# Kernel tuning notes

Measured on AMD Instinct MI355X. Metric: run time of the kernel, lower is better.

The kernel has to match this reference:

```python
import jax, jax.numpy as jnp
import numpy as np

N_NODES = 50000
N_EDGES = 600000
IN_DIM = 128
LATENT = 128
OUT_DIM = 40
NUM_LAYERS = 2


def setup_inputs() -> dict:
    key = jax.random.key(0)
    ks = jax.random.split(key, 8)
    nodes_feats = jax.random.normal(ks[0], (N_NODES, IN_DIM), dtype=jnp.float32)
    adj_list = jax.random.randint(ks[1], (N_EDGES, 2), 0, N_NODES, dtype=jnp.int64)
    s_in = 1.0 / np.sqrt(IN_DIM)
    s_cb = 1.0 / np.sqrt(2 * LATENT)
    s_out = 1.0 / np.sqrt(LATENT)
    W_in = jax.random.uniform(ks[2], (IN_DIM, LATENT), jnp.float32, -s_in, s_in)
    b_in = jnp.zeros((LATENT,), jnp.float32)
    W_comb = jax.random.uniform(ks[3], (NUM_LAYERS, 2 * LATENT, LATENT), jnp.float32, -s_cb, s_cb)
    b_comb = jnp.zeros((NUM_LAYERS, LATENT), jnp.float32)
    W_out = jax.random.uniform(ks[4], (LATENT, OUT_DIM), jnp.float32, -s_out, s_out)
    b_out = jnp.zeros((OUT_DIM,), jnp.float32)
    return {"nodes_feats": nodes_feats, "adj_list": adj_list, "W_in": W_in, "b_in": b_in,
            "W_comb": W_comb, "b_comb": b_comb, "W_out": W_out, "b_out": b_out}


def reference(nodes_feats, adj_list, W_in, b_in, W_comb, b_comb, W_out, b_out):
    n = nodes_feats.shape[0]
    fro = adj_list[:, 0]
    to = adj_list[:, 1]
    # initialize: project input features to latent space
    h = jax.nn.relu(nodes_feats @ W_in + b_in)  # [N, LATENT]
    # in-degree for mean aggregation (replaces per-node Python stack+mean)
    deg = jax.ops.segment_sum(jnp.ones(fro.shape[0], h.dtype), to, num_segments=n)
    inv_deg = 1.0 / jnp.maximum(deg, 1.0)  # guard isolated nodes
    for l in range(W_comb.shape[0]):
        # gather neighbor feats along edges, scatter-add to destinations, mean
        msg = jax.ops.segment_sum(h[fro], to, num_segments=n) * inv_deg[:, None]
        # combine: ReLU(Linear([node || message]))
        h = jax.nn.relu(jnp.concatenate([h, msg], axis=-1) @ W_comb[l] + b_comb[l])
    # output head (logits for CrossEntropyLoss)
    return h @ W_out + b_out
```

## Files before the change

### kernel.cpp

```cpp
#include <hip/hip_runtime.h>
#include <hip/hip_fp16.h>

#define N_NODES 50000
#define N_EDGES 600000
#define NBLK 49

typedef unsigned int u32;
typedef _Float16 v8h __attribute__((ext_vector_type(8)));
typedef _Float16 v4h __attribute__((ext_vector_type(4)));
typedef float v4f __attribute__((ext_vector_type(4)));

__device__ __forceinline__ float2 h2f2(u32 u) {
    __half2 h = *(__half2*)&u;
    return __half22float2(h);
}

__device__ __forceinline__ int calc_mode(const int* __restrict__ adj_w) {
    int l = threadIdx.x & 63;
    unsigned long long b = __ballot(adj_w[2 * l + 1] != 0);
    return (b == 0ull) ? 1 : 0;
}
__device__ __forceinline__ void load_edge(const int* __restrict__ a, int m, int e,
                                          int& fro, int& to) {
    if (m) {
        uint4 v = ((const uint4*)a)[e];
        fro = (int)v.x;
        to = (int)v.z;
    } else {
        uint2 v = ((const uint2*)a)[e];
        fro = (int)v.x;
        to = (int)v.y;
    }
}

#define CNT_B   293
#define WPREP_B 344
#define IN_B    1563

__global__ void k_count_prep(const int* __restrict__ adj_w, int* __restrict__ deg,
                             int* __restrict__ rank,
                             const float* __restrict__ W_in,
                             const float* __restrict__ W_comb,
                             const float* __restrict__ W_out,
                             _Float16* __restrict__ WinT,
                             _Float16* __restrict__ WcombT,
                             _Float16* __restrict__ WoutT) {
    if (blockIdx.x < CNT_B) {
        int m = calc_mode(adj_w);
        int base = blockIdx.x * 2048 + threadIdx.x;
        int to[8], r[8];
#pragma unroll
        for (int i = 0; i < 8; i++) {
            int e = base + i * 256;
            if (e < N_EDGES) {
                int f;
                load_edge(adj_w, m, e, f, to[i]);
            } else {
                to[i] = -1;
            }
        }
#pragma unroll
        for (int i = 0; i < 8; i++)
            if (to[i] >= 0) r[i] = atomicAdd(&deg[to[i]], 1);
#pragma unroll
        for (int i = 0; i < 8; i++) {
            int e = base + i * 256;
            if (e < N_EDGES) rank[e] = r[i];
        }
        return;
    }
    int idx = (blockIdx.x - CNT_B) * 256 + threadIdx.x;
    if (idx < 16384) {
        int n = idx & 127, k = idx >> 7;
        WinT[n * 128 + k] = (_Float16)W_in[k * 128 + n];
    } else if (idx < 16384 + 65536) {
        int j = idx - 16384;
        int l = j >> 15, r = j & 32767;
        int n = r & 127, k = r >> 7;
        WcombT[l * 32768 + n * 256 + k] = (_Float16)W_comb[l * 32768 + k * 128 + n];
    } else if (idx < 16384 + 65536 + 6144) {
        int j = idx - 81920;
        int n = j >> 7, k = j & 127;
        WoutT[n * 128 + k] = (n < 40) ? (_Float16)W_out[k * 40 + n] : (_Float16)0.f;
    }
}

__global__ void k_scan(const int* __restrict__ deg, int* __restrict__ row_ptr,
                       float* __restrict__ inv_deg, int* __restrict__ bsync) {
    __shared__ int s[1024];
    __shared__ int sbase;
    const int tid = threadIdx.x, b = blockIdx.x;
    const int i = b * 1024 + tid;
    int v = (i < N_NODES) ? deg[i] : 0;
    s[tid] = v;
    __syncthreads();
    for (int off = 1; off < 1024; off <<= 1) {
        int t = (tid >= off) ? s[tid - off] : 0;
        __syncthreads();
        s[tid] += t;
        __syncthreads();
    }
    if (tid == 1023)
        __hip_atomic_store(&bsync[b], 0x40000000 | s[1023], __ATOMIC_RELEASE,
                           __HIP_MEMORY_SCOPE_AGENT);
    if (tid < 64) {
        int acc = 0;
        if (tid < b) {
            int x;
            do {
                x = __hip_atomic_load(&bsync[tid], __ATOMIC_ACQUIRE,
                                      __HIP_MEMORY_SCOPE_AGENT);
            } while (x < 0x40000000);
            acc = x & 0x3fffffff;
        }
#pragma unroll
        for (int off = 32; off > 0; off >>= 1) acc += __shfl_down(acc, off);
        if (tid == 0) sbase = acc;
    }
    __syncthreads();
    if (i < N_NODES) {
        row_ptr[i] = sbase + s[tid] - v;
        inv_deg[i] = 1.0f / fmaxf((float)v, 1.0f);
    }
    if (i == 0) row_ptr[N_NODES] = N_EDGES;
}

__global__ __launch_bounds__(256, 2) void k_fill_in(const int* __restrict__ adj_w,
                                                    const int* __restrict__ row_ptr,
                                                    const int* __restrict__ rank,
                                                    int* __restrict__ edge_src,
                                                    const float* __restrict__ X,
                                                    const _Float16* __restrict__ WT,
                                                    const float* __restrict__ bias,
                                                    _Float16* __restrict__ h) {
    __shared__ __align__(16) _Float16 xs[32][136];
    if (blockIdx.x < CNT_B) {
        int m = calc_mode(adj_w);
        int base = blockIdx.x * 2048 + threadIdx.x;
        int to[8], fro[8], rk[8];
#pragma unroll
        for (int i = 0; i < 8; i++) {
            int e = base + i * 256;
            if (e < N_EDGES) {
                load_edge(adj_w, m, e, fro[i], to[i]);
                rk[i] = rank[e];
            } else {
                to[i] = -1;
            }
        }
#pragma unroll
        for (int i = 0; i < 8; i++)
            if (to[i] >= 0) edge_src[row_ptr[to[i]] + rk[i]] = fro[i];
        return;
    }
    const int t0 = threadIdx.x, w = t0 >> 6, l = t0 & 63;
    const int R0 = (blockIdx.x - CNT_B) * 32;
    const float4* X4 = (const float4*)X;
#pragma unroll
    for (int i = 0; i < 4; i++) {
        int idx = i * 256 + t0;
        int row = idx >> 5, c4 = idx & 31;
        int rr = R0 + row;
        if (rr > N_NODES - 1) rr = N_NODES - 1;
        float4 v = X4[(size_t)rr * 32 + c4];
        v4h hv = {(_Float16)v.x, (_Float16)v.y, (_Float16)v.z, (_Float16)v.w};
        *(v4h*)&xs[row][c4 * 4] = hv;
    }
    const int ch = w & 1, rh = w >> 1;
    v8h wf[4][4];
#pragma unroll
    for (int t = 0; t < 4; t++)
#pragma unroll
        for (int s = 0; s < 4; s++) {
            int n = ch * 64 + t * 16 + (l & 15);
            int k = s * 32 + (l >> 4) * 8;
            wf[t][s] = *(const v8h*)&WT[n * 128 + k];
        }
    v4f acc[4];
#pragma unroll
    for (int t = 0; t < 4; t++) acc[t] = (v4f){0.f, 0.f, 0.f, 0.f};
    __syncthreads();
#pragma unroll
    for (int s = 0; s < 4; s++) {
        v8h a = *(const v8h*)&xs[rh * 16 + (l & 15)][s * 32 + (l >> 4) * 8];
#pragma unroll
        for (int t = 0; t < 4; t++)
            acc[t] = __builtin_amdgcn_mfma_f32_16x16x32_f16(a, wf[t][s], acc[t], 0, 0, 0);
    }
#pragma unroll
    for (int t = 0; t < 4; t++) {
        int col = ch * 64 + t * 16 + (l & 15);
        float b = bias[col];
#pragma unroll
        for (int i = 0; i < 4; i++) {
            int row = R0 + rh * 16 + (l >> 4) * 4 + i;
            if (row < N_NODES)
                h[(size_t)row * 128 + col] = (_Float16)fmaxf(acc[t][i] + b, 0.f);
        }
    }
}

__global__ __launch_bounds__(256) void k_gather(const uint4* __restrict__ h16,
                                                uint4* __restrict__ msg16,
                                                const int* __restrict__ row_ptr,
                                                const int* __restrict__ edge_src,
                                                const float* __restrict__ inv_deg) {
    const int w = threadIdx.x >> 6, l = threadIdx.x & 63;
    const int grp = l >> 4, c = l & 15;
    const int wid = blockIdx.x * 4 + w, nw = gridDim.x * 4;
    if (wid >= N_NODES) return;
    int pe0 = row_ptr[wid], pe1 = row_ptr[wid + 1];
    for (int row = wid; row < N_NODES; row += nw) {
        const int e0 = pe0, e1 = pe1;
        const float inv = inv_deg[row];
        const int nrow = row + nw;
        if (nrow < N_NODES) {
            pe0 = row_ptr[nrow];
            pe1 = row_ptr[nrow + 1];
        }
        float a[8];
#pragma unroll
        for (int k = 0; k < 8; k++) a[k] = 0.f;
        for (int bse = e0; bse < e1; bse += 16) {
            uint4 v[4];
            int ok[4];
#pragma unroll
            for (int i = 0; i < 4; i++) {
                int ee = bse + 4 * i + grp;
                ok[i] = (ee < e1);
                int idx = ok[i] ? ee : (e1 - 1);
                v[i] = h16[(size_t)edge_src[idx] * 16 + c];
            }
#pragma unroll
            for (int i = 0; i < 4; i++) {
                if (ok[i]) {
                    u32 u[4] = {v[i].x, v[i].y, v[i].z, v[i].w};
#pragma unroll
                    for (int k = 0; k < 4; k++) {
                        float2 f = h2f2(u[k]);
                        a[2 * k] += f.x;
                        a[2 * k + 1] += f.y;
                    }
                }
            }
        }
#pragma unroll
        for (int k = 0; k < 8; k++) {
            a[k] += __shfl_xor(a[k], 16);
            a[k] += __shfl_xor(a[k], 32);
        }
        if (grp == 0) {
            __half2 o0 = __floats2half2_rn(a[0] * inv, a[1] * inv);
            __half2 o1 = __floats2half2_rn(a[2] * inv, a[3] * inv);
            __half2 o2 = __floats2half2_rn(a[4] * inv, a[5] * inv);
            __half2 o3 = __floats2half2_rn(a[6] * inv, a[7] * inv);
            uint4 o;
            o.x = *(u32*)&o0;
            o.y = *(u32*)&o1;
            o.z = *(u32*)&o2;
            o.w = *(u32*)&o3;
            msg16[(size_t)row * 16 + c] = o;
        }
    }
}

__global__ __launch_bounds__(256, 2) void k_layer(const _Float16* __restrict__ hin,
                                                  const _Float16* __restrict__ msg,
                                                  const _Float16* __restrict__ WT,
                                                  const float* __restrict__ bias,
                                                  _Float16* __restrict__ hout) {
    __shared__ __align__(16) _Float16 xs[64][264];
    const int t0 = threadIdx.x, w = t0 >> 6, l = t0 & 63;
    const int R0 = blockIdx.x * 64;
    const uint4* h4 = (const uint4*)hin;
    const uint4* m4 = (const uint4*)msg;
#pragma unroll
    for (int i = 0; i < 8; i++) {
        int idx = i * 256 + t0;
        int row = idx >> 5, c16 = idx & 31;
        int rr = R0 + row;
        if (rr > N_NODES - 1) rr = N_NODES - 1;
        uint4 v = (c16 < 16) ? h4[(size_t)rr * 16 + c16] : m4[(size_t)rr * 16 + (c16 - 16)];
        *(uint4*)&xs[row][c16 * 8] = v;
    }
    const int ch = w & 1, rh = w >> 1;
    v8h wf[4][8];
#pragma unroll
    for (int t = 0; t < 4; t++)
#pragma unroll
        for (int s = 0; s < 8; s++) {
            int n = ch * 64 + t * 16 + (l & 15);
            int k = s * 32 + (l >> 4) * 8;
            wf[t][s] = *(const v8h*)&WT[n * 256 + k];
        }
    v4f acc[2][4];
#pragma unroll
    for (int sub = 0; sub < 2; sub++)
#pragma unroll
        for (int t = 0; t < 4; t++) acc[sub][t] = (v4f){0.f, 0.f, 0.f, 0.f};
    __syncthreads();
#pragma unroll
    for (int s = 0; s < 8; s++) {
#pragma unroll
        for (int sub = 0; sub < 2; sub++) {
            v8h a = *(const v8h*)&xs[rh * 32 + sub * 16 + (l & 15)][s * 32 + (l >> 4) * 8];
#pragma unroll
            for (int t = 0; t < 4; t++)
                acc[sub][t] = __builtin_amdgcn_mfma_f32_16x16x32_f16(a, wf[t][s], acc[sub][t], 0, 0, 0);
        }
    }
#pragma unroll
    for (int sub = 0; sub < 2; sub++)
#pragma unroll
        for (int t = 0; t < 4; t++) {
            int col = ch * 64 + t * 16 + (l & 15);
            float b = bias[col];
#pragma unroll
            for (int i = 0; i < 4; i++) {
                int row = R0 + rh * 32 + sub * 16 + (l >> 4) * 4 + i;
                if (row < N_NODES)
                    hout[(size_t)row * 128 + col] = (_Float16)fmaxf(acc[sub][t][i] + b, 0.f);
            }
        }
}

__global__ __launch_bounds__(256, 2) void k_layer_out(const _Float16* __restrict__ hin,
                                                      const _Float16* __restrict__ msg,
                                                      const _Float16* __restrict__ WT,
                                                      const float* __restrict__ bias,
                                                      const _Float16* __restrict__ WoT,
                                                      const float* __restrict__ bias_o,
                                                      float* __restrict__ outp) {
    __shared__ __align__(16) _Float16 xs[64][264];
    const int t0 = threadIdx.x, w = t0 >> 6, l = t0 & 63;
    const int R0 = blockIdx.x * 64;
    const uint4* h4 = (const uint4*)hin;
    const uint4* m4 = (const uint4*)msg;
#pragma unroll
    for (int i = 0; i < 8; i++) {
        int idx = i * 256 + t0;
        int row = idx >> 5, c16 = idx & 31;
        int rr = R0 + row;
        if (rr > N_NODES - 1) rr = N_NODES - 1;
        uint4 v = (c16 < 16) ? h4[(size_t)rr * 16 + c16] : m4[(size_t)rr * 16 + (c16 - 16)];
        *(uint4*)&xs[row][c16 * 8] = v;
    }
    const int ch = w & 1, rh = w >> 1;
    v8h wf[4][8];
#pragma unroll
    for (int t = 0; t < 4; t++)
#pragma unroll
        for (int s = 0; s < 8; s++) {
            int n = ch * 64 + t * 16 + (l & 15);
            int k = s * 32 + (l >> 4) * 8;
            wf[t][s] = *(const v8h*)&WT[n * 256 + k];
        }
    v4f acc[2][4];
#pragma unroll
    for (int sub = 0; sub < 2; sub++)
#pragma unroll
        for (int t = 0; t < 4; t++) acc[sub][t] = (v4f){0.f, 0.f, 0.f, 0.f};
    __syncthreads();
#pragma unroll
    for (int s = 0; s < 8; s++) {
#pragma unroll
        for (int sub = 0; sub < 2; sub++) {
            v8h a = *(const v8h*)&xs[rh * 32 + sub * 16 + (l & 15)][s * 32 + (l >> 4) * 8];
#pragma unroll
            for (int t = 0; t < 4; t++)
                acc[sub][t] = __builtin_amdgcn_mfma_f32_16x16x32_f16(a, wf[t][s], acc[sub][t], 0, 0, 0);
        }
    }
    __syncthreads();
    _Float16* hs = &xs[0][0];
#pragma unroll
    for (int sub = 0; sub < 2; sub++)
#pragma unroll
        for (int t = 0; t < 4; t++) {
            int col = ch * 64 + t * 16 + (l & 15);
            float b = bias[col];
#pragma unroll
            for (int i = 0; i < 4; i++) {
                int lrow = rh * 32 + sub * 16 + (l >> 4) * 4 + i;
                hs[lrow * 136 + col] = (_Float16)fmaxf(acc[sub][t][i] + b, 0.f);
            }
        }
    v8h wo[3][4];
#pragma unroll
    for (int t = 0; t < 3; t++)
#pragma unroll
        for (int s = 0; s < 4; s++) {
            int n = t * 16 + (l & 15);
            int k = s * 32 + (l >> 4) * 8;
            wo[t][s] = *(const v8h*)&WoT[n * 128 + k];
        }
    v4f acc2[3];
#pragma unroll
    for (int t = 0; t < 3; t++) acc2[t] = (v4f){0.f, 0.f, 0.f, 0.f};
    __syncthreads();
#pragma unroll
    for (int s = 0; s < 4; s++) {
        v8h a = *(const v8h*)&hs[(w * 16 + (l & 15)) * 136 + s * 32 + (l >> 4) * 8];
#pragma unroll
        for (int t = 0; t < 3; t++)
            acc2[t] = __builtin_amdgcn_mfma_f32_16x16x32_f16(a, wo[t][s], acc2[t], 0, 0, 0);
    }
#pragma unroll
    for (int t = 0; t < 3; t++) {
        int col = t * 16 + (l & 15);
        if (col < 40) {
            float b = bias_o[col];
#pragma unroll
            for (int i = 0; i < 4; i++) {
                int row = R0 + w * 16 + (l >> 4) * 4 + i;
                if (row < N_NODES) outp[(size_t)row * 40 + col] = acc2[t][i] + b;
            }
        }
    }
}

extern "C" void kernel_launch(void* const* d_in, const int* in_sizes, int n_in,
                              void* d_out, int out_size, void* d_ws, size_t ws_size,
                              hipStream_t stream) {
    int ix[8] = {0, 1, 2, 3, 4, 5, 6, 7};
    int tmp[8] = {-1, -1, -1, -1, -1, -1, -1, -1};
    for (int i = 0; i < n_in && i < 8; i++) {
        switch (in_sizes[i]) {
            case 6400000: tmp[0] = i; break;
            case 1200000: case 2400000: tmp[1] = i; break;
            case 16384:   tmp[2] = i; break;
            case 128:     tmp[3] = i; break;
            case 65536:   tmp[4] = i; break;
            case 256:     tmp[5] = i; break;
            case 5120:    tmp[6] = i; break;
            case 40:      tmp[7] = i; break;
        }
    }
    int found = 0;
    for (int j = 0; j < 8; j++) found += (tmp[j] >= 0);
    if (found == 8) for (int j = 0; j < 8; j++) ix[j] = tmp[j];

    const float* X      = (const float*)d_in[ix[0]];
    const int*   adj_w  = (const int*)d_in[ix[1]];
    const float* W_in   = (const float*)d_in[ix[2]];
    const float* b_in   = (const float*)d_in[ix[3]];
    const float* W_comb = (const float*)d_in[ix[4]];
    const float* b_comb = (const float*)d_in[ix[5]];
    const float* W_out  = (const float*)d_in[ix[6]];
    const float* b_out  = (const float*)d_in[ix[7]];
    float* out = (float*)d_out;

    char* base = (char*)d_ws;
    int*      deg      = (int*)(base + 0);
    int*      bsync    = (int*)(base + 200000);
    int*      row_ptr  = (int*)(base + 200256);
    int*      rank     = (int*)(base + 400272);
    float*    inv_deg  = (float*)(base + 2800272);
    int*      edge_src = (int*)(base + 3000272);
    _Float16* WinT     = (_Float16*)(base + 5400272);
    _Float16* WcombT   = (_Float16*)(base + 5433040);
    _Float16* WoutT    = (_Float16*)(base + 5564112);
    _Float16* hA       = (_Float16*)(base + 5576448);
    _Float16* hB       = (_Float16*)(base + 18376448);
    _Float16* msg      = (_Float16*)(base + 31176448);

    hipMemsetAsync(deg, 0, 200256, stream);
    k_count_prep<<<CNT_B + WPREP_B, 256, 0, stream>>>(adj_w, deg, rank, W_in, W_comb, W_out,
                                                      WinT, WcombT, WoutT);
    k_scan<<<NBLK, 1024, 0, stream>>>(deg, row_ptr, inv_deg, bsync);
    k_fill_in<<<CNT_B + IN_B, 256, 0, stream>>>(adj_w, row_ptr, rank, edge_src,
                                                X, WinT, b_in, hA);

    k_gather<<<2048, 256, 0, stream>>>((const uint4*)hA, (uint4*)msg, row_ptr, edge_src, inv_deg);
    k_layer<<<782, 256, 0, stream>>>(hA, msg, WcombT, b_comb, hB);

    k_gather<<<2048, 256, 0, stream>>>((const uint4*)hB, (uint4*)msg, row_ptr, edge_src, inv_deg);
    k_layer_out<<<782, 256, 0, stream>>>(hB, msg, WcombT + 32768, b_comb + 128,
                                         WoutT, b_out, out);
}
```

Before: 242.5 us.

## Fuse neighbor mean-gather into combine layer kernels via shared-memory tile

The separate gather kernel, which wrote the aggregated message to global memory, is removed. Each combine-layer block now gathers neighbor features for its own 64 rows straight into the second half of its shared-memory input tile before the MFMA matmul. This saves the message write and re-read plus two kernel launches. In exchange, the gather runs with only 782 blocks, and each 16-lane group walks one row's edge list serially in steps of 4, which may lower memory-level parallelism and load balance compared with the old 2048-block gather kernel.

```diff
diff --git a/kernel.cpp b/kernel.cpp
--- a/kernel.cpp
+++ b/kernel.cpp
@@ -200,36 +200,27 @@
     }
 }
 
-__global__ __launch_bounds__(256) void k_gather(const uint4* __restrict__ h16,
-                                                uint4* __restrict__ msg16,
-                                                const int* __restrict__ row_ptr,
-                                                const int* __restrict__ edge_src,
-                                                const float* __restrict__ inv_deg) {
-    const int w = threadIdx.x >> 6, l = threadIdx.x & 63;
-    const int grp = l >> 4, c = l & 15;
-    const int wid = blockIdx.x * 4 + w, nw = gridDim.x * 4;
-    if (wid >= N_NODES) return;
-    int pe0 = row_ptr[wid], pe1 = row_ptr[wid + 1];
-    for (int row = wid; row < N_NODES; row += nw) {
-        const int e0 = pe0, e1 = pe1;
-        const float inv = inv_deg[row];
-        const int nrow = row + nw;
-        if (nrow < N_NODES) {
-            pe0 = row_ptr[nrow];
-            pe1 = row_ptr[nrow + 1];
-        }
+__device__ __forceinline__ void gather_tile(_Float16 (*xs)[264], const int* rp,
+                                            const float* sinv, const uint4* __restrict__ hh,
+                                            const int* __restrict__ edge_src,
+                                            int w, int l) {
+    const int g = l >> 4, c = l & 15;
+#pragma unroll
+    for (int j = 0; j < 4; j++) {
+        int lrow = w * 16 + g * 4 + j;
+        int e0 = rp[lrow], e1 = rp[lrow + 1];
         float a[8];
 #pragma unroll
         for (int k = 0; k < 8; k++) a[k] = 0.f;
-        for (int bse = e0; bse < e1; bse += 16) {
+        for (int bse = e0; bse < e1; bse += 4) {
             uint4 v[4];
             int ok[4];
 #pragma unroll
             for (int i = 0; i < 4; i++) {
-                int ee = bse + 4 * i + grp;
+                int ee = bse + i;
                 ok[i] = (ee < e1);
                 int idx = ok[i] ? ee : (e1 - 1);
-                v[i] = h16[(size_t)edge_src[idx] * 16 + c];
+                v[i] = hh[(size_t)edge_src[idx] * 16 + c];
             }
 #pragma unroll
             for (int i = 0; i < 4; i++) {
@@ -244,45 +235,52 @@
                 }
             }
         }
-#pragma unroll
-        for (int k = 0; k < 8; k++) {
-            a[k] += __shfl_xor(a[k], 16);
-            a[k] += __shfl_xor(a[k], 32);
-        }
-        if (grp == 0) {
-            __half2 o0 = __floats2half2_rn(a[0] * inv, a[1] * inv);
-            __half2 o1 = __floats2half2_rn(a[2] * inv, a[3] * inv);
-            __half2 o2 = __floats2half2_rn(a[4] * inv, a[5] * inv);
-            __half2 o3 = __floats2half2_rn(a[6] * inv, a[7] * inv);
-            uint4 o;
-            o.x = *(u32*)&o0;
-            o.y = *(u32*)&o1;
-            o.z = *(u32*)&o2;
-            o.w = *(u32*)&o3;
-            msg16[(size_t)row * 16 + c] = o;
-        }
+        const float inv = sinv[lrow];
+        __half2 o0 = __floats2half2_rn(a[0] * inv, a[1] * inv);
+        __half2 o1 = __floats2half2_rn(a[2] * inv, a[3] * inv);
+        __half2 o2 = __floats2half2_rn(a[4] * inv, a[5] * inv);
+        __half2 o3 = __floats2half2_rn(a[6] * inv, a[7] * inv);
+        uint4 o;
+        o.x = *(u32*)&o0;
+        o.y = *(u32*)&o1;
+        o.z = *(u32*)&o2;
+        o.w = *(u32*)&o3;
+        *(uint4*)&xs[lrow][128 + c * 8] = o;
     }
 }
 
 __global__ __launch_bounds__(256, 2) void k_layer(const _Float16* __restrict__ hin,
-                                                  const _Float16* __restrict__ msg,
                                                   const _Float16* __restrict__ WT,
                                                   const float* __restrict__ bias,
+                                                  const int* __restrict__ row_ptr,
+                                                  const int* __restrict__ edge_src,
+                                                  const float* __restrict__ inv_deg,
                                                   _Float16* __restrict__ hout) {
     __shared__ __align__(16) _Float16 xs[64][264];
+    __shared__ int rp[65];
+    __shared__ float sinv[64];
     const int t0 = threadIdx.x, w = t0 >> 6, l = t0 & 63;
     const int R0 = blockIdx.x * 64;
+    if (t0 < 65) {
+        int rr = R0 + t0;
+        if (rr > N_NODES) rr = N_NODES;
+        rp[t0] = row_ptr[rr];
+    } else if (t0 >= 128 && t0 < 192) {
+        int rr = R0 + (t0 - 128);
+        if (rr > N_NODES - 1) rr = N_NODES - 1;
+        sinv[t0 - 128] = inv_deg[rr];
+    }
     const uint4* h4 = (const uint4*)hin;
-    const uint4* m4 = (const uint4*)msg;
-#pragma unroll
-    for (int i = 0; i < 8; i++) {
+#pragma unroll
+    for (int i = 0; i < 4; i++) {
         int idx = i * 256 + t0;
-        int row = idx >> 5, c16 = idx & 31;
+        int row = idx >> 4, c16 = idx & 15;
         int rr = R0 + row;
         if (rr > N_NODES - 1) rr = N_NODES - 1;
-        uint4 v = (c16 < 16) ? h4[(size_t)rr * 16 + c16] : m4[(size_t)rr * 16 + (c16 - 16)];
-        *(uint4*)&xs[row][c16 * 8] = v;
-    }
+        *(uint4*)&xs[row][c16 * 8] = h4[(size_t)rr * 16 + c16];
+    }
+    __syncthreads();
+    gather_tile(xs, rp, sinv, h4, edge_src, w, l);
     const int ch = w & 1, rh = w >> 1;
     v8h wf[4][8];
 #pragma unroll
@@ -325,26 +323,39 @@
 }
 
 __global__ __launch_bounds__(256, 2) void k_layer_out(const _Float16* __restrict__ hin,
-                                                      const _Float16* __restrict__ msg,
                                                       const _Float16* __restrict__ WT,
                                                       const float* __restrict__ bias,
+                                                      const int* __restrict__ row_ptr,
+                                                      const int* __restrict__ edge_src,
+                                                      const float* __restrict__ inv_deg,
                                                       const _Float16* __restrict__ WoT,
                                                       const float* __restrict__ bias_o,
                                                       float* __restrict__ outp) {
     __shared__ __align__(16) _Float16 xs[64][264];
+    __shared__ int rp[65];
+    __shared__ float sinv[64];
     const int t0 = threadIdx.x, w = t0 >> 6, l = t0 & 63;
     const int R0 = blockIdx.x * 64;
+    if (t0 < 65) {
+        int rr = R0 + t0;
+        if (rr > N_NODES) rr = N_NODES;
+        rp[t0] = row_ptr[rr];
+    } else if (t0 >= 128 && t0 < 192) {
+        int rr = R0 + (t0 - 128);
+        if (rr > N_NODES - 1) rr = N_NODES - 1;
+        sinv[t0 - 128] = inv_deg[rr];
+    }
     const uint4* h4 = (const uint4*)hin;
-    const uint4* m4 = (const uint4*)msg;
-#pragma unroll
-    for (int i = 0; i < 8; i++) {
+#pragma unroll
+    for (int i = 0; i < 4; i++) {
         int idx = i * 256 + t0;
-        int row = idx >> 5, c16 = idx & 31;
+        int row = idx >> 4, c16 = idx & 15;
         int rr = R0 + row;
         if (rr > N_NODES - 1) rr = N_NODES - 1;
-        uint4 v = (c16 < 16) ? h4[(size_t)rr * 16 + c16] : m4[(size_t)rr * 16 + (c16 - 16)];
-        *(uint4*)&xs[row][c16 * 8] = v;
-    }
+        *(uint4*)&xs[row][c16 * 8] = h4[(size_t)rr * 16 + c16];
+    }
+    __syncthreads();
+    gather_tile(xs, rp, sinv, h4, edge_src, w, l);
     const int ch = w & 1, rh = w >> 1;
     v8h wf[4][8];
 #pragma unroll
@@ -462,7 +473,6 @@
     _Float16* WoutT    = (_Float16*)(base + 5564112);
     _Float16* hA       = (_Float16*)(base + 5576448);
     _Float16* hB       = (_Float16*)(base + 18376448);
-    _Float16* msg      = (_Float16*)(base + 31176448);
 
     hipMemsetAsync(deg, 0, 200256, stream);
     k_count_prep<<<CNT_B + WPREP_B, 256, 0, stream>>>(adj_w, deg, rank, W_in, W_comb, W_out,
@@ -471,10 +481,7 @@
     k_fill_in<<<CNT_B + IN_B, 256, 0, stream>>>(adj_w, row_ptr, rank, edge_src,
                                                 X, WinT, b_in, hA);
 
-    k_gather<<<2048, 256, 0, stream>>>((const uint4*)hA, (uint4*)msg, row_ptr, edge_src, inv_deg);
-    k_layer<<<782, 256, 0, stream>>>(hA, msg, WcombT, b_comb, hB);
-
-    k_gather<<<2048, 256, 0, stream>>>((const uint4*)hB, (uint4*)msg, row_ptr, edge_src, inv_deg);
-    k_layer_out<<<782, 256, 0, stream>>>(hB, msg, WcombT + 32768, b_comb + 128,
-                                         WoutT, b_out, out);
-}
+    k_layer<<<782, 256, 0, stream>>>(hA, WcombT, b_comb, row_ptr, edge_src, inv_deg, hB);
+    k_layer_out<<<782, 256, 0, stream>>>(hB, WcombT + 32768, b_comb + 128,
+                                         row_ptr, edge_src, inv_deg, WoutT, b_out, out);
+}
```

Result: slower. 280.0 us (+15.5%).
